# Performance work log

Measured on AMD Instinct MI355X. Metric: run time of the kernel, lower is better.

The kernel has to match this reference:

```python
import jax, jax.numpy as jnp
import numpy as np

N_HEADS = 16
N_EMBED = 1024
HEAD = N_EMBED // N_HEADS
NEG = -1e10


def setup_inputs() -> dict:
    key = jax.random.key(0)
    ks = jax.random.split(key, 12)
    B, Tq, Tk, C = 4, 2048, 2048, N_EMBED
    s = 1.0 / np.sqrt(C)
    return {
        "x": jax.random.normal(ks[0], (B, Tq, C), jnp.float32),
        "features": jax.random.normal(ks[1], (B, Tk, C), jnp.float32),
        "mask": jax.random.randint(ks[2], (B, 1, 1, Tk), 0, 2, jnp.int32),
        "wq": jax.random.normal(ks[3], (C, C), jnp.float32) * s,
        "bq": jnp.zeros((C,), jnp.float32),
        "wk": jax.random.normal(ks[4], (C, C), jnp.float32) * s,
        "bk": jnp.zeros((C,), jnp.float32),
        "wv": jax.random.normal(ks[5], (C, C), jnp.float32) * s,
        "bv": jnp.zeros((C,), jnp.float32),
        "wo": jax.random.normal(ks[6], (C, C), jnp.float32) * s,
        "bo": jnp.zeros((C,), jnp.float32),
    }


def reference(x, features, mask, wq, bq, wk, bk, wv, bv, wo, bo):
    B, Tq, C = x.shape
    Tk = features.shape[1]
    # project and split heads: [B, H, T, Dh]
    q = (x @ wq + bq).reshape(B, Tq, N_HEADS, HEAD).transpose(0, 2, 1, 3)
    k = (features @ wk + bk).reshape(B, Tk, N_HEADS, HEAD).transpose(0, 2, 1, 3)
    v = (features @ wv + bv).reshape(B, Tk, N_HEADS, HEAD).transpose(0, 2, 1, 3)
    attn = jnp.einsum("bhqd,bhkd->bhqk", q, k) / np.sqrt(HEAD)
    attn = jnp.where(mask == 0, NEG, attn)
    attn = jax.nn.softmax(attn, axis=-1)  # dropout p=0 (eval)
    out = jnp.einsum("bhqk,bhkd->bhqd", attn, v)
    out = out.transpose(0, 2, 1, 3).reshape(B, Tq, C)
    return out @ wo + bo
```

## Files before the change

### kernel.cpp

```cpp
#include <hip/hip_runtime.h>
#include <stdint.h>
#include <type_traits>

typedef __attribute__((ext_vector_type(8))) short bf16x8;
typedef __attribute__((ext_vector_type(4))) float f32x4;
typedef __attribute__((ext_vector_type(16))) float f32x16;

#define BB 4
#define NH 16
#define TT 2048
#define HD 64
#define CC 1024

__device__ __forceinline__ unsigned short f2bf(float f) {
  unsigned int u = __builtin_bit_cast(unsigned int, f);
  u += 0x7fff + ((u >> 16) & 1);
  return (unsigned short)(u >> 16);
}

__device__ __forceinline__ float fast_exp2(float x) {
#if __has_builtin(__builtin_amdgcn_exp2f)
  return __builtin_amdgcn_exp2f(x);
#else
  return exp2f(x);
#endif
}

__device__ __forceinline__ unsigned int cvtpk(float lo, float hi) {
  unsigned int r;
  asm("v_cvt_pk_bf16_f32 %0, %1, %2" : "=v"(r) : "v"(lo), "v"(hi));
  return r;
}

__device__ __forceinline__ void plswap(unsigned int& a, unsigned int& b) {
#if __has_builtin(__builtin_amdgcn_permlane32_swap)
  auto r = __builtin_amdgcn_permlane32_swap(a, b, false, false);
  a = r[0];
  b = r[1];
#else
  unsigned int as = __shfl_xor((int)a, 32), bs = __shfl_xor((int)b, 32);
  bool hi = (threadIdx.x & 32) != 0;
  unsigned int na = hi ? bs : a;
  unsigned int nb = hi ? b : as;
  a = na; b = nb;
#endif
}

__device__ __forceinline__ float partner32(float x, bool hi) {
  unsigned int a = __builtin_bit_cast(unsigned int, x), b = a;
  plswap(a, b);
  return __builtin_bit_cast(float, hi ? a : b);
}

__device__ __forceinline__ void g2l16(const void* g, void* s) {
  __builtin_amdgcn_global_load_lds(
      (const __attribute__((address_space(1))) unsigned int*)g,
      (__attribute__((address_space(3))) unsigned int*)s, 16, 0, 0);
}

__global__ __launch_bounds__(256) void cast2(
    const float* __restrict__ x, const float* __restrict__ ft,
    unsigned short* __restrict__ xb, unsigned short* __restrict__ fb, int n) {
  const float* in = blockIdx.y ? ft : x;
  unsigned short* out = blockIdx.y ? fb : xb;
  int i = (blockIdx.x * 256 + threadIdx.x) * 4;
  if (i >= n) return;
  float4 v = *(const float4*)(in + i);
  ushort4 o;
  o.x = f2bf(v.x); o.y = f2bf(v.y); o.z = f2bf(v.z); o.w = f2bf(v.w);
  *(ushort4*)(out + i) = o;
}

__global__ __launch_bounds__(256) void make_m01(
    const int* __restrict__ mask, float* __restrict__ m01, int n) {
  int i = blockIdx.x * 256 + threadIdx.x;
  if (i < n) m01[i] = mask[i] ? 1.0f : 0.0f;
}

__global__ __launch_bounds__(256) void transpose_cast_w4(
    const float* __restrict__ wq, const float* __restrict__ wk,
    const float* __restrict__ wv, const float* __restrict__ wo,
    unsigned short* __restrict__ wqkvt, unsigned short* __restrict__ wot) {
  __shared__ float tile[32][33];
  const int z = blockIdx.z;
  const float* w = (z == 0) ? wq : (z == 1) ? wk : (z == 2) ? wv : wo;
  unsigned short* wt = (z < 3) ? wqkvt + (size_t)z * CC * CC : wot;
  int nb = blockIdx.x * 32, kb = blockIdx.y * 32;
  int tx = threadIdx.x, ty = threadIdx.y;
#pragma unroll
  for (int r = ty; r < 32; r += 8)
    tile[r][tx] = w[(size_t)(kb + r) * CC + nb + tx];
  __syncthreads();
#pragma unroll
  for (int r = ty; r < 32; r += 8)
    wt[(size_t)(nb + r) * CC + kb + tx] = f2bf(tile[tx][r]);
}

__global__ __launch_bounds__(256) void gemm_qkv(
    const unsigned short* __restrict__ xb, const unsigned short* __restrict__ fb,
    const unsigned short* __restrict__ Wt,
    const float* __restrict__ bq, const float* __restrict__ bk,
    const float* __restrict__ bv, const float* __restrict__ m01,
    unsigned short* __restrict__ Qb, unsigned short* __restrict__ Kb,
    unsigned short* __restrict__ Vtb, float qscale) {
  __shared__ unsigned short As[128 * 64];
  __shared__ unsigned short Bs[128 * 64];
  int lin = blockIdx.y * gridDim.x + blockIdx.x;
  int cpx = (gridDim.x * gridDim.y) >> 3;
  int sw = (lin & 7) * cpx + (lin >> 3);
  const int n0g = (sw % 24) * 128;
  const int m0 = (sw / 24) * 128;
  const int sec = n0g >> 10;
  const int n0 = n0g & (CC - 1);
  const unsigned short* A = (sec == 0) ? xb : fb;
  const unsigned short* Bt = Wt + (size_t)n0g * CC;

  const int t = threadIdx.x, l = t & 63, w = t >> 6;
  const int lr = l & 15, lg = l >> 4;
  const int wr = w >> 1, wc = w & 1;

  const int sR = t >> 3;
  const int sx = ((t & 7) * 16) ^ ((sR & 7) << 4);
  const unsigned short* gA = A + (size_t)(m0 + sR) * CC + (sx >> 1);
  const unsigned short* gB = Bt + (size_t)sR * CC + (sx >> 1);
  auto stage = [&]() {
#pragma unroll
    for (int i = 0; i < 4; ++i) {
      g2l16(gA + (size_t)(i * 32) * CC, (char*)As + t * 16 + i * 4096);
      g2l16(gB + (size_t)(i * 32) * CC, (char*)Bs + t * 16 + i * 4096);
    }
    gA += 64; gB += 64;
  };

  const int axs = (lr & 7) << 4;
  const int col0 = (lg * 16) ^ axs;
  const int col1 = (64 + lg * 16) ^ axs;
  const int abase = (wr * 64 + lr) * 128;
  const int bbase = (wc * 64 + lr) * 128;

  f32x4 acc[4][4] = {};
  for (int j = 0; j < 16; ++j) {
    stage();
    asm volatile("s_waitcnt vmcnt(0)" ::: "memory");
    __syncthreads();
    bf16x8 af[4], bfr[4];
#pragma unroll
    for (int mi = 0; mi < 4; ++mi)
      af[mi] = *(const bf16x8*)((const char*)As + abase + mi * 2048 + col0);
#pragma unroll
    for (int nj = 0; nj < 4; ++nj)
      bfr[nj] = *(const bf16x8*)((const char*)Bs + bbase + nj * 2048 + col0);
#pragma unroll
    for (int mi = 0; mi < 4; ++mi)
#pragma unroll
      for (int nj = 0; nj < 4; ++nj)
        acc[mi][nj] = __builtin_amdgcn_mfma_f32_16x16x32_bf16(
            af[mi], bfr[nj], acc[mi][nj], 0, 0, 0);
#pragma unroll
    for (int mi = 0; mi < 4; ++mi)
      af[mi] = *(const bf16x8*)((const char*)As + abase + mi * 2048 + col1);
#pragma unroll
    for (int nj = 0; nj < 4; ++nj)
      bfr[nj] = *(const bf16x8*)((const char*)Bs + bbase + nj * 2048 + col1);
#pragma unroll
    for (int mi = 0; mi < 4; ++mi)
#pragma unroll
      for (int nj = 0; nj < 4; ++nj)
        acc[mi][nj] = __builtin_amdgcn_mfma_f32_16x16x32_bf16(
            af[mi], bfr[nj], acc[mi][nj], 0, 0, 0);
    __syncthreads();
  }

  const float* bp = (sec == 0) ? bq : (sec == 1) ? bk : bv;
  const float scale = (sec == 0) ? qscale : 1.0f;
#pragma unroll
  for (int mi = 0; mi < 4; ++mi) {
#pragma unroll
    for (int nj = 0; nj < 4; ++nj) {
      int col = n0 + wc * 64 + nj * 16 + lr;
      float bias = bp[col];
#pragma unroll
      for (int j = 0; j < 4; ++j) {
        int rowm = m0 + wr * 64 + mi * 16 + lg * 4 + j;
        float v = (acc[mi][nj][j] + bias) * scale;
        int b_ = rowm >> 11, tq = rowm & (TT - 1);
        int h_ = col >> 6, d_ = col & (HD - 1);
        if (sec < 2) {
          unsigned short* dst = (sec == 0) ? Qb : Kb;
          dst[((size_t)((b_ * NH + h_) * TT + tq) << 6) + d_] = f2bf(v);
        } else {
          v *= m01[rowm];
          Vtb[((size_t)((b_ * NH + h_) * HD + d_) * TT) + tq] = f2bf(v);
        }
      }
    }
  }
}

__global__ __launch_bounds__(256) void gemm_out(
    const unsigned short* __restrict__ A, const unsigned short* __restrict__ Bt,
    const float* __restrict__ bias, float* __restrict__ Out) {
  __shared__ unsigned short As[128 * 64];
  __shared__ unsigned short Bs[128 * 64];
  int lin = blockIdx.y * gridDim.x + blockIdx.x;
  int cpx = (gridDim.x * gridDim.y) >> 3;
  int sw = (lin & 7) * cpx + (lin >> 3);
  const int n0 = (sw % 8) * 128;
  const int m0 = (sw / 8) * 128;
  const int t = threadIdx.x, l = t & 63, w = t >> 6;
  const int lr = l & 15, lg = l >> 4;
  const int wr = w >> 1, wc = w & 1;

  const int sR = t >> 3;
  const int sx = ((t & 7) * 16) ^ ((sR & 7) << 4);
  const unsigned short* gA = A + (size_t)(m0 + sR) * CC + (sx >> 1);
  const unsigned short* gB = Bt + (size_t)(n0 + sR) * CC + (sx >> 1);
  auto stage = [&]() {
#pragma unroll
    for (int i = 0; i < 4; ++i) {
      g2l16(gA + (size_t)(i * 32) * CC, (char*)As + t * 16 + i * 4096);
      g2l16(gB + (size_t)(i * 32) * CC, (char*)Bs + t * 16 + i * 4096);
    }
    gA += 64; gB += 64;
  };

  const int axs = (lr & 7) << 4;
  const int col0 = (lg * 16) ^ axs;
  const int col1 = (64 + lg * 16) ^ axs;
  const int abase = (wr * 64 + lr) * 128;
  const int bbase = (wc * 64 + lr) * 128;

  f32x4 acc[4][4] = {};
  for (int j = 0; j < 16; ++j) {
    stage();
    asm volatile("s_waitcnt vmcnt(0)" ::: "memory");
    __syncthreads();
    bf16x8 af[4], bfr[4];
#pragma unroll
    for (int mi = 0; mi < 4; ++mi)
      af[mi] = *(const bf16x8*)((const char*)As + abase + mi * 2048 + col0);
#pragma unroll
    for (int nj = 0; nj < 4; ++nj)
      bfr[nj] = *(const bf16x8*)((const char*)Bs + bbase + nj * 2048 + col0);
#pragma unroll
    for (int mi = 0; mi < 4; ++mi)
#pragma unroll
      for (int nj = 0; nj < 4; ++nj)
        acc[mi][nj] = __builtin_amdgcn_mfma_f32_16x16x32_bf16(
            af[mi], bfr[nj], acc[mi][nj], 0, 0, 0);
#pragma unroll
    for (int mi = 0; mi < 4; ++mi)
      af[mi] = *(const bf16x8*)((const char*)As + abase + mi * 2048 + col1);
#pragma unroll
    for (int nj = 0; nj < 4; ++nj)
      bfr[nj] = *(const bf16x8*)((const char*)Bs + bbase + nj * 2048 + col1);
#pragma unroll
    for (int mi = 0; mi < 4; ++mi)
#pragma unroll
      for (int nj = 0; nj < 4; ++nj)
        acc[mi][nj] = __builtin_amdgcn_mfma_f32_16x16x32_bf16(
            af[mi], bfr[nj], acc[mi][nj], 0, 0, 0);
    __syncthreads();
  }

#pragma unroll
  for (int mi = 0; mi < 4; ++mi) {
#pragma unroll
    for (int nj = 0; nj < 4; ++nj) {
      int col = n0 + wc * 64 + nj * 16 + lr;
      float bv = bias[col];
#pragma unroll
      for (int j = 0; j < 4; ++j) {
        int rowm = m0 + wr * 64 + mi * 16 + lg * 4 + j;
        Out[(size_t)rowm * CC + col] = acc[mi][nj][j] + bv;
      }
    }
  }
}

__global__ __launch_bounds__(256) void attn_fwd8(
    const unsigned short* __restrict__ Q, const unsigned short* __restrict__ K,
    const unsigned short* __restrict__ Vt, const float* __restrict__ m01,
    unsigned short* __restrict__ O) {
  __shared__ __attribute__((aligned(64))) char ldsb[40960];
  const int t = threadIdx.x, l = t & 63, w = t >> 6;
  const int q5 = l & 31, hig = l >> 5;
  const bool hib = hig != 0;
  int lin = blockIdx.y * gridDim.x + blockIdx.x;
  int sw = (lin & 7) * 128 + (lin >> 3);
  const int bx = sw & 15, bh = sw >> 4;
  const int b_ = bh >> 4, h_ = bh & (NH - 1);
  const int q = bx * 128 + w * 32 + q5;
  const size_t base = (size_t)bh * TT * HD;
  const unsigned short* Kg = K + base;
  const unsigned short* Vg = Vt + (size_t)bh * HD * TT;

  bf16x8 qf[4];
  {
    const unsigned short* qp = Q + base + (size_t)q * HD + 8 * hig;
#pragma unroll
    for (int dk = 0; dk < 4; ++dk) qf[dk] = *(const bf16x8*)(qp + dk * 16);
  }

  int ka[4];
  {
    int swz = (q5 & 7) << 4;
#pragma unroll
    for (int dk = 0; dk < 4; ++dk)
      ka[dk] = q5 * 128 + ((dk * 32 + hig * 16) ^ swz);
  }
  int moff = 32768 + hig * 16;

  const int s1 = t + 256;
  const int r0 = t >> 3, c0 = (t & 7) * 16, x0 = c0 ^ ((r0 & 7) << 4);
  const int r1 = s1 >> 3, c1 = (s1 & 7) * 16, x1 = c1 ^ ((r1 & 7) << 4);
  const unsigned short* gk0 = Kg + r0 * HD + (x0 >> 1);
  const unsigned short* gk1 = Kg + r1 * HD + (x1 >> 1);
  const unsigned short* gv0 = Vg + (size_t)r0 * TT + (x0 >> 1);
  const unsigned short* gv1 = Vg + (size_t)r1 * TT + (x1 >> 1);

  auto stage = [&](int boff) {
    g2l16(gk0, ldsb + t * 16 + boff);
    g2l16(gk1, ldsb + t * 16 + 4096 + boff);
    g2l16(gv0, ldsb + 16384 + t * 16 + boff);
    g2l16(gv1, ldsb + 16384 + t * 16 + 4096 + boff);
    gk0 += 4096; gk1 += 4096; gv0 += 64; gv1 += 64;
  };

  f32x16 ot[2];
#pragma unroll
  for (int i = 0; i < 16; ++i) { ot[0][i] = 0.f; ot[1][i] = 0.f; }
  float l0 = 0.f, l1 = 0.f, l2 = 0.f, l3 = 0.f;

  {
    const float* mg = m01 + (size_t)b_ * TT;
#pragma unroll
    for (int i = 0; i < 2; ++i) {
      int s = t + i * 256;
      g2l16(mg + s * 4, ldsb + 32768 + s * 16);
    }
  }
  stage(0);
  asm volatile("s_waitcnt vmcnt(0)" ::: "memory");
  __syncthreads();

  auto compute = [&](auto Bc) {
    constexpr int BO = decltype(Bc)::value;
    constexpr int MO = BO ? 256 : 0;
    f32x16 s[2] = {};
    __builtin_amdgcn_s_setprio(1);
#pragma unroll
    for (int dk = 0; dk < 4; ++dk) {
      bf16x8 kf0 = *(const bf16x8*)(ldsb + ka[dk] + BO);
      bf16x8 kf1 = *(const bf16x8*)(ldsb + ka[dk] + 4096 + BO);
      s[0] = __builtin_amdgcn_mfma_f32_32x32x16_bf16(kf0, qf[dk], s[0], 0, 0, 0);
      s[1] = __builtin_amdgcn_mfma_f32_32x32x16_bf16(kf1, qf[dk], s[1], 0, 0, 0);
    }
    __builtin_amdgcn_s_setprio(0);

    unsigned int wl[2][4], wh[2][4];
#pragma unroll
    for (int kk = 0; kk < 2; ++kk)
#pragma unroll
      for (int g = 0; g < 4; ++g) {
        int i = g * 4;
        float e0 = fast_exp2(s[kk][i + 0]);
        float e1 = fast_exp2(s[kk][i + 1]);
        float e2 = fast_exp2(s[kk][i + 2]);
        float e3 = fast_exp2(s[kk][i + 3]);
        f32x4 mk = *(const f32x4*)(ldsb + moff + MO + kk * 128 + g * 32);
        l0 = fmaf(e0, mk[0], l0);
        l1 = fmaf(e1, mk[1], l1);
        l2 = fmaf(e2, mk[2], l2);
        l3 = fmaf(e3, mk[3], l3);
        wl[kk][g] = cvtpk(e0, e1);
        wh[kk][g] = cvtpk(e2, e3);
      }

    bf16x8 pa[4];
#pragma unroll
    for (int ks = 0; ks < 4; ++ks) {
      const int kk = ks >> 1, gA = 2 * (ks & 1), gB = gA + 1;
      unsigned int a0 = wl[kk][gA], b0 = wl[kk][gB];
      unsigned int a1 = wh[kk][gA], b1 = wh[kk][gB];
      plswap(a0, b0);
      plswap(a1, b1);
      unsigned int pw[4] = {a0, a1, b0, b1};
      pa[ks] = *(bf16x8*)pw;
    }

    __builtin_amdgcn_s_setprio(1);
#pragma unroll
    for (int ks = 0; ks < 4; ++ks) {
      bf16x8 vf0 = *(const bf16x8*)(ldsb + ka[ks] + 16384 + BO);
      bf16x8 vf1 = *(const bf16x8*)(ldsb + ka[ks] + 16384 + 4096 + BO);
      ot[0] = __builtin_amdgcn_mfma_f32_32x32x16_bf16(vf0, pa[ks], ot[0], 0, 0, 0);
      ot[1] = __builtin_amdgcn_mfma_f32_32x32x16_bf16(vf1, pa[ks], ot[1], 0, 0, 0);
    }
    __builtin_amdgcn_s_setprio(0);
  };

  for (int j = 0; j < 16; ++j) {
    stage(8192);
    compute(std::integral_constant<int, 0>{});
    asm volatile("s_waitcnt vmcnt(0)" ::: "memory");
    __syncthreads();
    if (j < 15) stage(0);
    compute(std::integral_constant<int, 8192>{});
    asm volatile("s_waitcnt vmcnt(0)" ::: "memory");
    __syncthreads();
    moff += 512;
  }

  float l_ = (l0 + l1) + (l2 + l3);
  float l_tot = l_ + partner32(l_, hib);
  const float inv = 1.f / l_tot;
  unsigned short* orow = O + ((size_t)(b_ * TT) + q) * CC + h_ * 64 + 4 * hig;
#pragma unroll
  for (int dt = 0; dt < 2; ++dt)
#pragma unroll
    for (int g = 0; g < 4; ++g) {
      unsigned short pk4[4];
#pragma unroll
      for (int j = 0; j < 4; ++j) pk4[j] = f2bf(ot[dt][4 * g + j] * inv);
      *(ushort4*)(orow + dt * 32 + 8 * g) = *(ushort4*)pk4;
    }
}

extern "C" void kernel_launch(void* const* d_in, const int* in_sizes, int n_in,
                              void* d_out, int out_size, void* d_ws, size_t ws_size,
                              hipStream_t stream) {
  const float* x  = (const float*)d_in[0];
  const float* ft = (const float*)d_in[1];
  const int* mask = (const int*)d_in[2];
  const float* wq = (const float*)d_in[3];
  const float* bq = (const float*)d_in[4];
  const float* wk = (const float*)d_in[5];
  const float* bk = (const float*)d_in[6];
  const float* wv = (const float*)d_in[7];
  const float* bv = (const float*)d_in[8];
  const float* wo = (const float*)d_in[9];
  const float* bo = (const float*)d_in[10];
  float* out = (float*)d_out;

  char* ws = (char*)d_ws;
  const size_t NTOK = (size_t)BB * TT;
  const size_t SB = NTOK * CC * 2;
  unsigned short* xb   = (unsigned short*)ws; ws += SB;
  unsigned short* fb   = (unsigned short*)ws; ws += SB;
  unsigned short* Qb   = (unsigned short*)ws; ws += SB;
  unsigned short* Kb   = (unsigned short*)ws; ws += SB;
  unsigned short* Vtb  = (unsigned short*)ws; ws += SB;
  unsigned short* AO   = (unsigned short*)ws; ws += SB;
  unsigned short* wqkvt = (unsigned short*)ws; ws += (size_t)3 * CC * CC * 2;
  unsigned short* wot   = (unsigned short*)ws; ws += (size_t)CC * CC * 2;
  float* m01 = (float*)ws; ws += NTOK * 4;

  int ncast = (int)(NTOK * CC);
  dim3 gc(ncast / 4 / 256, 2);
  cast2<<<gc, 256, 0, stream>>>(x, ft, xb, fb, ncast);
  dim3 tb(32, 8), tg(32, 32, 4);
  transpose_cast_w4<<<tg, tb, 0, stream>>>(wq, wk, wv, wo, wqkvt, wot);
  make_m01<<<(int)(NTOK / 256), 256, 0, stream>>>(mask, m01, (int)NTOK);

  const float qscale = 0.125f * 1.44269504f;
  dim3 gq(24, 64);
  gemm_qkv<<<gq, 256, 0, stream>>>(xb, fb, wqkvt, bq, bk, bv, m01,
                                   Qb, Kb, Vtb, qscale);

  dim3 ga(16, 64);
  attn_fwd8<<<ga, 256, 0, stream>>>(Qb, Kb, Vtb, m01, AO);

  dim3 go(8, 64);
  gemm_out<<<go, 256, 0, stream>>>(AO, wot, bo, out);
}
```

Baseline: 237.1 us.

## Halve QKV GEMM K-tile to 32 and vectorize transposed V stores

The QKV projection GEMM now stages a K-depth of 32 per iteration instead of 64, with a new 4-way XOR swizzle, halving LDS use per block so more blocks can be resident. The price is twice as many loop iterations and barriers. The epilogue is split by section, and the V path loads four mask values at once and writes four consecutive tokens as one packed 8-byte store instead of scattered 2-byte stores.

```diff
diff --git a/kernel.cpp b/kernel.cpp
--- a/kernel.cpp
+++ b/kernel.cpp
@@ -103,8 +103,8 @@
     const float* __restrict__ bv, const float* __restrict__ m01,
     unsigned short* __restrict__ Qb, unsigned short* __restrict__ Kb,
     unsigned short* __restrict__ Vtb, float qscale) {
-  __shared__ unsigned short As[128 * 64];
-  __shared__ unsigned short Bs[128 * 64];
+  __shared__ unsigned short As[128 * 32];
+  __shared__ unsigned short Bs[128 * 32];
   int lin = blockIdx.y * gridDim.x + blockIdx.x;
   int cpx = (gridDim.x * gridDim.y) >> 3;
   int sw = (lin & 7) * cpx + (lin >> 3);
@@ -119,79 +119,83 @@
   const int lr = l & 15, lg = l >> 4;
   const int wr = w >> 1, wc = w & 1;
 
-  const int sR = t >> 3;
-  const int sx = ((t & 7) * 16) ^ ((sR & 7) << 4);
-  const unsigned short* gA = A + (size_t)(m0 + sR) * CC + (sx >> 1);
-  const unsigned short* gB = Bt + (size_t)sR * CC + (sx >> 1);
+  const int c1 = t + 256;
+  const int r0 = t >> 2, k0e = (((t & 3) ^ (r0 & 3)) * 8);
+  const int r1 = c1 >> 2, k1e = (((c1 & 3) ^ (r1 & 3)) * 8);
+  const unsigned short* gA0 = A + (size_t)(m0 + r0) * CC + k0e;
+  const unsigned short* gA1 = A + (size_t)(m0 + r1) * CC + k1e;
+  const unsigned short* gB0 = Bt + (size_t)r0 * CC + k0e;
+  const unsigned short* gB1 = Bt + (size_t)r1 * CC + k1e;
   auto stage = [&]() {
-#pragma unroll
-    for (int i = 0; i < 4; ++i) {
-      g2l16(gA + (size_t)(i * 32) * CC, (char*)As + t * 16 + i * 4096);
-      g2l16(gB + (size_t)(i * 32) * CC, (char*)Bs + t * 16 + i * 4096);
-    }
-    gA += 64; gB += 64;
+    g2l16(gA0, (char*)As + t * 16);
+    g2l16(gA1, (char*)As + t * 16 + 4096);
+    g2l16(gB0, (char*)Bs + t * 16);
+    g2l16(gB1, (char*)Bs + t * 16 + 4096);
+    gA0 += 32; gA1 += 32; gB0 += 32; gB1 += 32;
   };
 
-  const int axs = (lr & 7) << 4;
-  const int col0 = (lg * 16) ^ axs;
-  const int col1 = (64 + lg * 16) ^ axs;
-  const int abase = (wr * 64 + lr) * 128;
-  const int bbase = (wc * 64 + lr) * 128;
+  const int colx = (lg * 16) ^ ((lr & 3) << 4);
+  const int abase = (wr * 64 + lr) * 64 + colx;
+  const int bbase = (wc * 64 + lr) * 64 + colx;
 
   f32x4 acc[4][4] = {};
-  for (int j = 0; j < 16; ++j) {
+  for (int j = 0; j < 32; ++j) {
     stage();
     asm volatile("s_waitcnt vmcnt(0)" ::: "memory");
     __syncthreads();
     bf16x8 af[4], bfr[4];
 #pragma unroll
     for (int mi = 0; mi < 4; ++mi)
-      af[mi] = *(const bf16x8*)((const char*)As + abase + mi * 2048 + col0);
+      af[mi] = *(const bf16x8*)((const char*)As + abase + mi * 1024);
 #pragma unroll
     for (int nj = 0; nj < 4; ++nj)
-      bfr[nj] = *(const bf16x8*)((const char*)Bs + bbase + nj * 2048 + col0);
+      bfr[nj] = *(const bf16x8*)((const char*)Bs + bbase + nj * 1024);
 #pragma unroll
     for (int mi = 0; mi < 4; ++mi)
 #pragma unroll
       for (int nj = 0; nj < 4; ++nj)
         acc[mi][nj] = __builtin_amdgcn_mfma_f32_16x16x32_bf16(
             af[mi], bfr[nj], acc[mi][nj], 0, 0, 0);
-#pragma unroll
-    for (int mi = 0; mi < 4; ++mi)
-      af[mi] = *(const bf16x8*)((const char*)As + abase + mi * 2048 + col1);
-#pragma unroll
-    for (int nj = 0; nj < 4; ++nj)
-      bfr[nj] = *(const bf16x8*)((const char*)Bs + bbase + nj * 2048 + col1);
-#pragma unroll
-    for (int mi = 0; mi < 4; ++mi)
-#pragma unroll
-      for (int nj = 0; nj < 4; ++nj)
-        acc[mi][nj] = __builtin_amdgcn_mfma_f32_16x16x32_bf16(
-            af[mi], bfr[nj], acc[mi][nj], 0, 0, 0);
-    __syncthreads();
-  }
-
-  const float* bp = (sec == 0) ? bq : (sec == 1) ? bk : bv;
-  const float scale = (sec == 0) ? qscale : 1.0f;
-#pragma unroll
-  for (int mi = 0; mi < 4; ++mi) {
-#pragma unroll
-    for (int nj = 0; nj < 4; ++nj) {
-      int col = n0 + wc * 64 + nj * 16 + lr;
-      float bias = bp[col];
-#pragma unroll
-      for (int j = 0; j < 4; ++j) {
-        int rowm = m0 + wr * 64 + mi * 16 + lg * 4 + j;
-        float v = (acc[mi][nj][j] + bias) * scale;
-        int b_ = rowm >> 11, tq = rowm & (TT - 1);
+    __syncthreads();
+  }
+
+  if (sec < 2) {
+    const float* bp = (sec == 0) ? bq : bk;
+    const float scale = (sec == 0) ? qscale : 1.0f;
+    unsigned short* dst = (sec == 0) ? Qb : Kb;
+#pragma unroll
+    for (int mi = 0; mi < 4; ++mi) {
+#pragma unroll
+      for (int nj = 0; nj < 4; ++nj) {
+        int col = n0 + wc * 64 + nj * 16 + lr;
+        float bias = bp[col];
+#pragma unroll
+        for (int j = 0; j < 4; ++j) {
+          int rowm = m0 + wr * 64 + mi * 16 + lg * 4 + j;
+          float v = (acc[mi][nj][j] + bias) * scale;
+          int b_ = rowm >> 11, tq = rowm & (TT - 1);
+          int h_ = col >> 6, d_ = col & (HD - 1);
+          dst[((size_t)((b_ * NH + h_) * TT + tq) << 6) + d_] = f2bf(v);
+        }
+      }
+    }
+  } else {
+#pragma unroll
+    for (int mi = 0; mi < 4; ++mi) {
+      int rowb = m0 + wr * 64 + mi * 16 + lg * 4;
+      int b_ = rowb >> 11, tq = rowb & (TT - 1);
+      f32x4 mv = *(const f32x4*)(m01 + rowb);
+#pragma unroll
+      for (int nj = 0; nj < 4; ++nj) {
+        int col = n0 + wc * 64 + nj * 16 + lr;
+        float bias = bv[col];
         int h_ = col >> 6, d_ = col & (HD - 1);
-        if (sec < 2) {
-          unsigned short* dst = (sec == 0) ? Qb : Kb;
-          dst[((size_t)((b_ * NH + h_) * TT + tq) << 6) + d_] = f2bf(v);
-        } else {
-          v *= m01[rowm];
-          Vtb[((size_t)((b_ * NH + h_) * HD + d_) * TT) + tq] = f2bf(v);
-        }
+        unsigned short pk[4];
+#pragma unroll
+        for (int j = 0; j < 4; ++j)
+          pk[j] = f2bf((acc[mi][nj][j] + bias) * mv[j]);
+        *(ushort4*)(Vtb + ((size_t)((b_ * NH + h_) * HD + d_) << 11) + tq) =
+            *(ushort4*)pk;
       }
     }
   }
```

After: 219.6 us. 7.4% less time.
